# Optimization experiments

Hardware: AMD Instinct MI355X
Metric: run time of the kernel (lower is better)

Reference implementation:

```python
import jax, jax.numpy as jnp
import numpy as np

NUM_CHANNELS = 64
IN_FEATURES = 256
OUT_FEATURES = 256
B = 128
N = 2048


def setup_inputs() -> dict:
    key = jax.random.key(0)
    k_x, k_c, k_w, k_b = jax.random.split(key, 4)
    x = jax.random.normal(k_x, (B, N, IN_FEATURES), dtype=jnp.float32)
    channels = jax.random.randint(k_c, (N,), 0, NUM_CHANNELS, dtype=jnp.int64)
    # kaiming_uniform_(a=sqrt(5)) over fan_in -> bound = 1/sqrt(fan_in)
    wb = 1.0 / np.sqrt(IN_FEATURES)
    weight = jax.random.uniform(k_w, (NUM_CHANNELS, OUT_FEATURES, IN_FEATURES),
                                dtype=jnp.float32, minval=-wb, maxval=wb)
    bias = jax.random.uniform(k_b, (NUM_CHANNELS, OUT_FEATURES),
                              dtype=jnp.float32, minval=-wb, maxval=wb)
    return {"x": x, "channels": channels, "weight": weight, "bias": bias}


def reference(x, channels, weight, bias):
    # Gather per-point weights/biases by channel id (shared across batch).
    w = weight[channels]          # [N, out, in]
    b = bias[channels]            # [N, out]
    # Equivalent to bmm over the point axis: [B,N,in] x [N,out,in] -> [B,N,out]
    y = jnp.einsum('bni,noi->bno', x, w)
    y = y + b                     # broadcast over batch
    y = jnp.tanh(y)               # activation=True
    y = y + x                     # residual mode 1 (out == in)
    return (y, channels)
```

## Files before the change

kernel.cpp:

```cpp
#include <hip/hip_runtime.h>
#include <hip/hip_bf16.h>


#define N_SZ  2048
#define CHUNK 8

typedef __attribute__((ext_vector_type(8))) __bf16 bf16x8;
typedef __attribute__((ext_vector_type(4))) float  f32x4;

__device__ __forceinline__ float bf2f(unsigned u16) {
    union { unsigned u; float f; } v; v.u = u16 << 16;
    return v.f;
}
__device__ __forceinline__ float tanh_fast(float s) {
    float a = fabsf(s);
    float t = __expf(-2.0f * a);
    float r = (1.0f - t) * __builtin_amdgcn_rcpf(1.0f + t);
    return __builtin_copysignf(r, s);
}
__device__ __forceinline__ bf16x8 cvt8(float4 a, float4 b) {
    bf16x8 v;
    v[0] = (__bf16)a.x; v[1] = (__bf16)a.y; v[2] = (__bf16)a.z; v[3] = (__bf16)a.w;
    v[4] = (__bf16)b.x; v[5] = (__bf16)b.y; v[6] = (__bf16)b.z; v[7] = (__bf16)b.w;
    return v;
}
__device__ __forceinline__ void wg_barrier_lds() {
    asm volatile("s_waitcnt lgkmcnt(0)" ::: "memory");
    __builtin_amdgcn_s_barrier();
    asm volatile("" ::: "memory");
}

__global__ __launch_bounds__(1024) void sort_kernel(const int* __restrict__ channels,
                                                    int* __restrict__ perm,
                                                    float* __restrict__ out_ch) {
    __shared__ int cnt[64], off[64];
    const int t = threadIdx.x;
    if (t < 64) cnt[t] = 0;
    __syncthreads();
    const int n0 = t, n1 = t + 1024;
    const int c0 = channels[n0], c1 = channels[n1];
    atomicAdd(&cnt[c0], 1);
    atomicAdd(&cnt[c1], 1);
    out_ch[n0] = (float)c0;
    out_ch[n1] = (float)c1;
    __syncthreads();
    if (t == 0) { int s = 0; for (int i = 0; i < 64; ++i) { off[i] = s; s += cnt[i]; } }
    __syncthreads();
    int p0 = atomicAdd(&off[c0], 1); perm[p0] = n0 | (c0 << 16);
    int p1 = atomicAdd(&off[c1], 1); perm[p1] = n1 | (c1 << 16);
}

__global__ __launch_bounds__(256) void wconv_kernel(const float* __restrict__ w,
                                                    unsigned short* __restrict__ wsW) {
    const size_t t = (size_t)blockIdx.x * 256 + threadIdx.x;
    const float* src = w + t * 8;
    float4 f0 = *(const float4*)(src);
    float4 f1 = *(const float4*)(src + 4);
    bf16x8 v = cvt8(f0, f1);
    *(bf16x8*)(wsW + t * 8) = v;
}

__global__ __launch_bounds__(512, 4) void channel_dense_kernel(
    const float* __restrict__ x, const int* __restrict__ perm,
    const unsigned short* __restrict__ wsW, const float* __restrict__ bias,
    float* __restrict__ y)
{
    __shared__ __align__(16) unsigned char sA[2][16384];

    const int g  = blockIdx.x;
    const int lg = (g & 7) * 128 + (g >> 3);
    const int chunk   = lg >> 2;
    const int quarter = lg & 3;
    const int tid  = threadIdx.x;
    const int lane = tid & 63, wv = tid >> 6;
    const int lr   = lane & 15, lg4 = lane >> 4;

    const int sr = tid >> 4;
    const int sh = tid & 15;
    const int s_slab = sh >> 1;
    const int s_lin0 = sr * 64 + (sh & 1) * 32;
    const int s_swz  = ((sr & 7) << 4) ^ ((s_slab & 3) << 4);
    const int s_addr0 = s_slab * 2048 + ((s_lin0)      ^ s_swz);
    const int s_addr1 = s_slab * 2048 + ((s_lin0 + 16) ^ s_swz);

    float4 la0, la1, la2, la3;
    auto stage_load = [&](int n_) {
        const float* p = x + ((size_t)(quarter * 32 + sr) * N_SZ + n_) * 256 + sh * 16;
        la0 = *(const float4*)(p);     la1 = *(const float4*)(p + 4);
        la2 = *(const float4*)(p + 8); la3 = *(const float4*)(p + 12);
    };
    auto stage_write = [&](int buf) {
        *(bf16x8*)(&sA[buf][s_addr0]) = cvt8(la0, la1);
        *(bf16x8*)(&sA[buf][s_addr1]) = cvt8(la2, la3);
    };

    const int p0 = chunk * CHUNK;

    int pv_cur = perm[p0];
    stage_load(pv_cur & 0xffff);
    stage_write(0);
    int pv_nxt = perm[p0 + 1];
    stage_load(pv_nxt & 0xffff);
    wg_barrier_lds();

    bf16x8 wreg[2][8];
    float4 bv0, bv1;
    int c_cur = -1;
    int cur = 0;
    const int o0 = wv * 32 + lg4 * 4;

    for (int i = 0; i < CHUNK; ++i) {
        const int n = pv_cur & 0xffff;
        const int c = pv_cur >> 16;
        if (c != c_cur) {
            c_cur = c;
            const unsigned short* wl = wsW + (((size_t)c * 256 + wv * 32 + lr) << 8) + lg4 * 8;
            #pragma unroll
            for (int kt = 0; kt < 8; ++kt) {
                wreg[0][kt] = *(const bf16x8*)(wl + kt * 32);
                wreg[1][kt] = *(const bf16x8*)(wl + 16 * 256 + kt * 32);
            }
            bv0 = *(const float4*)(bias + c * 256 + o0);
            bv1 = *(const float4*)(bias + c * 256 + o0 + 16);
        }

        f32x4 acc[2][2] = {};
        #pragma unroll
        for (int kt = 0; kt < 8; ++kt) {
            const int lb = (lr * 64 + lg4 * 16) ^ ((lr & 7) << 4) ^ ((kt & 3) << 4);
            bf16x8 xf0 = *(const bf16x8*)(&sA[cur][kt * 2048 + lb]);
            bf16x8 xf1 = *(const bf16x8*)(&sA[cur][kt * 2048 + 1024 + lb]);
            acc[0][0] = __builtin_amdgcn_mfma_f32_16x16x32_bf16(wreg[0][kt], xf0, acc[0][0], 0, 0, 0);
            acc[0][1] = __builtin_amdgcn_mfma_f32_16x16x32_bf16(wreg[0][kt], xf1, acc[0][1], 0, 0, 0);
            acc[1][0] = __builtin_amdgcn_mfma_f32_16x16x32_bf16(wreg[1][kt], xf0, acc[1][0], 0, 0, 0);
            acc[1][1] = __builtin_amdgcn_mfma_f32_16x16x32_bf16(wreg[1][kt], xf1, acc[1][1], 0, 0, 0);
        }

        if (i < CHUNK - 1) {
            stage_write(cur ^ 1);
            if (i < CHUNK - 2) {
                pv_cur = pv_nxt;
                pv_nxt = perm[p0 + i + 2];
                stage_load(pv_nxt & 0xffff);
            } else {
                pv_cur = pv_nxt;
            }
        }

        #pragma unroll
        for (int mo = 0; mo < 2; ++mo) {
            const float4 bv = mo ? bv1 : bv0;
            const int oo    = o0 + mo * 16;
            const int s     = oo >> 5;
            const int intra = (oo & 31) * 2;
            #pragma unroll
            for (int nb = 0; nb < 2; ++nb) {
                const int rl = nb * 16 + lr;
                const int b  = quarter * 32 + rl;
                const int rbyte = s * 2048 +
                    ((rl * 64 + intra) ^ ((rl & 7) << 4) ^ ((s & 3) << 4));
                uint2 rv = *(const uint2*)(&sA[cur][rbyte]);
                float4 o;
                o.x = tanh_fast(acc[mo][nb][0] + bv.x) + bf2f(rv.x & 0xffffu);
                o.y = tanh_fast(acc[mo][nb][1] + bv.y) + bf2f(rv.x >> 16);
                o.z = tanh_fast(acc[mo][nb][2] + bv.z) + bf2f(rv.y & 0xffffu);
                o.w = tanh_fast(acc[mo][nb][3] + bv.w) + bf2f(rv.y >> 16);
                *(float4*)(y + ((size_t)b * N_SZ + n) * 256 + oo) = o;
            }
        }

        if (i < CHUNK - 1) wg_barrier_lds();
        cur ^= 1;
    }
}

extern "C" void kernel_launch(void* const* d_in, const int* in_sizes, int n_in,
                              void* d_out, int out_size, void* d_ws, size_t ws_size,
                              hipStream_t stream) {
    const float* x        = (const float*)d_in[0];
    const int*   channels = (const int*)d_in[1];
    const float* weight   = (const float*)d_in[2];
    const float* bias     = (const float*)d_in[3];
    float* y = (float*)d_out;

    unsigned short* wsW = (unsigned short*)d_ws;
    int* perm = (int*)((unsigned char*)d_ws + (64u << 17));

    sort_kernel<<<dim3(1), dim3(1024), 0, stream>>>(
        channels, perm, y + (size_t)128 * N_SZ * 256);
    wconv_kernel<<<dim3(2048), dim3(256), 0, stream>>>(weight, wsW);
    channel_dense_kernel<<<dim3(1024), dim3(512), 0, stream>>>(
        x, perm, wsW, bias, y);
}
```

Baseline: 191.3 us.

## Drop channel sort; process contiguous points with per-point weight prefetch

Removes the single-block sort kernel and the permutation indirection. Each block now walks 16 contiguous points instead of 8 sorted ones, with half as many blocks. Because points are no longer grouped by channel, the weights and bias for the next point are reloaded every iteration and overlapped with the staging of the next x tile. This saves the serial sort launch and makes the x and y accesses contiguous, but it adds a weight reload from L2 per point instead of reuse across same-channel points, and leaves fewer blocks in the grid.

```diff
diff --git a/kernel.cpp b/kernel.cpp
--- a/kernel.cpp
+++ b/kernel.cpp
@@ -3,7 +3,7 @@
 
 
 #define N_SZ  2048
-#define CHUNK 8
+#define CH    16
 
 typedef __attribute__((ext_vector_type(8))) __bf16 bf16x8;
 typedef __attribute__((ext_vector_type(4))) float  f32x4;
@@ -30,26 +30,6 @@
     asm volatile("" ::: "memory");
 }
 
-__global__ __launch_bounds__(1024) void sort_kernel(const int* __restrict__ channels,
-                                                    int* __restrict__ perm,
-                                                    float* __restrict__ out_ch) {
-    __shared__ int cnt[64], off[64];
-    const int t = threadIdx.x;
-    if (t < 64) cnt[t] = 0;
-    __syncthreads();
-    const int n0 = t, n1 = t + 1024;
-    const int c0 = channels[n0], c1 = channels[n1];
-    atomicAdd(&cnt[c0], 1);
-    atomicAdd(&cnt[c1], 1);
-    out_ch[n0] = (float)c0;
-    out_ch[n1] = (float)c1;
-    __syncthreads();
-    if (t == 0) { int s = 0; for (int i = 0; i < 64; ++i) { off[i] = s; s += cnt[i]; } }
-    __syncthreads();
-    int p0 = atomicAdd(&off[c0], 1); perm[p0] = n0 | (c0 << 16);
-    int p1 = atomicAdd(&off[c1], 1); perm[p1] = n1 | (c1 << 16);
-}
-
 __global__ __launch_bounds__(256) void wconv_kernel(const float* __restrict__ w,
                                                     unsigned short* __restrict__ wsW) {
     const size_t t = (size_t)blockIdx.x * 256 + threadIdx.x;
@@ -61,17 +41,19 @@
 }
 
 __global__ __launch_bounds__(512, 4) void channel_dense_kernel(
-    const float* __restrict__ x, const int* __restrict__ perm,
+    const float* __restrict__ x, const int* __restrict__ channels,
     const unsigned short* __restrict__ wsW, const float* __restrict__ bias,
     float* __restrict__ y)
 {
     __shared__ __align__(16) unsigned char sA[2][16384];
 
-    const int g  = blockIdx.x;
-    const int lg = (g & 7) * 128 + (g >> 3);
-    const int chunk   = lg >> 2;
-    const int quarter = lg & 3;
-    const int tid  = threadIdx.x;
+    const int g   = blockIdx.x;
+    const int xcd = g & 7;
+    const int t8  = g >> 3;
+    const int quarter = t8 & 3;
+    const int chunk   = xcd * 16 + (t8 >> 2);
+    const int n0  = chunk * CH;
+    const int tid = threadIdx.x;
     const int lane = tid & 63, wv = tid >> 6;
     const int lr   = lane & 15, lg4 = lane >> 4;
 
@@ -94,35 +76,38 @@
         *(bf16x8*)(&sA[buf][s_addr1]) = cvt8(la2, la3);
     };
 
-    const int p0 = chunk * CHUNK;
+    bf16x8 wreg[2][8];
+    float4 bv0, bv1;
+    const int o0 = wv * 32 + lg4 * 4;
 
-    int pv_cur = perm[p0];
-    stage_load(pv_cur & 0xffff);
+    auto load_w = [&](int c_) {
+        const unsigned short* wl = wsW + (((size_t)c_ * 256 + wv * 32 + lr) << 8) + lg4 * 8;
+        #pragma unroll
+        for (int kt = 0; kt < 8; ++kt) {
+            wreg[0][kt] = *(const bf16x8*)(wl + kt * 32);
+            wreg[1][kt] = *(const bf16x8*)(wl + 16 * 256 + kt * 32);
+        }
+    };
+    auto load_bias = [&](int c_) {
+        bv0 = *(const float4*)(bias + c_ * 256 + o0);
+        bv1 = *(const float4*)(bias + c_ * 256 + o0 + 16);
+    };
+
+    int c_cur = channels[n0];
+    load_w(c_cur);
+    load_bias(c_cur);
+    stage_load(n0);
     stage_write(0);
-    int pv_nxt = perm[p0 + 1];
-    stage_load(pv_nxt & 0xffff);
+    stage_load(n0 + 1);
     wg_barrier_lds();
 
-    bf16x8 wreg[2][8];
-    float4 bv0, bv1;
-    int c_cur = -1;
     int cur = 0;
-    const int o0 = wv * 32 + lg4 * 4;
 
-    for (int i = 0; i < CHUNK; ++i) {
-        const int n = pv_cur & 0xffff;
-        const int c = pv_cur >> 16;
-        if (c != c_cur) {
-            c_cur = c;
-            const unsigned short* wl = wsW + (((size_t)c * 256 + wv * 32 + lr) << 8) + lg4 * 8;
-            #pragma unroll
-            for (int kt = 0; kt < 8; ++kt) {
-                wreg[0][kt] = *(const bf16x8*)(wl + kt * 32);
-                wreg[1][kt] = *(const bf16x8*)(wl + 16 * 256 + kt * 32);
-            }
-            bv0 = *(const float4*)(bias + c * 256 + o0);
-            bv1 = *(const float4*)(bias + c * 256 + o0 + 16);
-        }
+    for (int i = 0; i < CH; ++i) {
+        const int n = n0 + i;
+        const bool more = (i < CH - 1);
+        int c_nxt = c_cur;
+        if (more) c_nxt = channels[n + 1];
 
         f32x4 acc[2][2] = {};
         #pragma unroll
@@ -136,15 +121,10 @@
             acc[1][1] = __builtin_amdgcn_mfma_f32_16x16x32_bf16(wreg[1][kt], xf1, acc[1][1], 0, 0, 0);
         }
 
-        if (i < CHUNK - 1) {
+        if (more) {
+            load_w(c_nxt);
             stage_write(cur ^ 1);
-            if (i < CHUNK - 2) {
-                pv_cur = pv_nxt;
-                pv_nxt = perm[p0 + i + 2];
-                stage_load(pv_nxt & 0xffff);
-            } else {
-                pv_cur = pv_nxt;
-            }
+            if (i < CH - 2) stage_load(n + 2);
         }
 
         #pragma unroll
@@ -169,9 +149,18 @@
             }
         }
 
-        if (i < CHUNK - 1) wg_barrier_lds();
+        if (more) {
+            load_bias(c_nxt);
+            wg_barrier_lds();
+        }
         cur ^= 1;
+        c_cur = c_nxt;
     }
+}
+
+__global__ void channels_copy_kernel(const int* __restrict__ ch, float* __restrict__ out) {
+    int i = blockIdx.x * 256 + threadIdx.x;
+    if (i < N_SZ) out[i] = (float)ch[i];
 }
 
 extern "C" void kernel_launch(void* const* d_in, const int* in_sizes, int n_in,
@@ -184,11 +173,10 @@
     float* y = (float*)d_out;
 
     unsigned short* wsW = (unsigned short*)d_ws;
-    int* perm = (int*)((unsigned char*)d_ws + (64u << 17));
 
-    sort_kernel<<<dim3(1), dim3(1024), 0, stream>>>(
-        channels, perm, y + (size_t)128 * N_SZ * 256);
     wconv_kernel<<<dim3(2048), dim3(256), 0, stream>>>(weight, wsW);
-    channel_dense_kernel<<<dim3(1024), dim3(512), 0, stream>>>(
-        x, perm, wsW, bias, y);
+    channel_dense_kernel<<<dim3(512), dim3(512), 0, stream>>>(
+        x, channels, wsW, bias, y);
+    channels_copy_kernel<<<dim3(N_SZ / 256), dim3(256), 0, stream>>>(
+        channels, y + (size_t)128 * N_SZ * 256);
 }
```

After: 233.3 us. 21.9% more time.
